# Optimization experiments

Hardware: AMD Instinct MI355X
Metric: run time of the kernel (lower is better)

The kernel has to match this reference:

```python
import jax, jax.numpy as jnp
import numpy as np

D = 64; H = 6; DH = 32; CB = 16; SB = 8; NSEL = 2; WIN = 7; OUT = 7; HID = 32
SCALE = DH ** -0.5
NEG = -3.4e38  # max_neg_value for fp32 masking


def _rope(x):
    # interleaved (lucidrains rotary-embedding-torch style), theta=10000
    n, d = x.shape[-2], x.shape[-1]
    inv = 1.0 / (10000.0 ** (jnp.arange(0, d, 2, dtype=jnp.float32) / d))
    fr = jnp.arange(n, dtype=jnp.float32)[:, None] * inv[None, :]  # n, d/2
    fr = jnp.repeat(fr, 2, axis=-1)                                # n, d
    c, s = jnp.cos(fr), jnp.sin(fr)
    xr = jnp.stack((-x[..., 1::2], x[..., 0::2]), axis=-1).reshape(x.shape)
    return x * c + xr * s


def reference(x, We, be, gamma, Wq, Wk, Wv, k_pos, v_pos, mem_k, mem_v,
              Wkc1, bkc1, Wkc2, bkc2, Wvc1, bvc1, Wvc2, bvc2,
              Wg, bg, Wo, Wh1, bh1, Wh2, bh2):
    B, N = x.shape
    nC = N // CB  # compressed blocks
    nF = N // SB  # fine/selection blocks

    # per-feature scalar embedding: Linear(1, 64)
    h = x[..., None] * We[0] + be  # B,N,D

    # RMSNorm (F.normalize * sqrt(D) * (gamma + 1))
    nrm = jnp.sqrt(jnp.sum(h * h, axis=-1, keepdims=True))
    hn = h / jnp.maximum(nrm, 1e-12) * jnp.sqrt(float(D)) * (gamma + 1.0)

    def proj(W):
        return jnp.einsum('bnd,de->bne', hn, W).reshape(B, N, H, DH).transpose(0, 2, 1, 3)
    q, k, v = proj(Wq), proj(Wk), proj(Wv)  # B,H,N,DH

    # ---- compressed branch (un-rotated q,k; intra-block pos emb + MLP compressor) ----
    kp = jnp.tile(k_pos, (1, nC, 1))  # H,N,DH
    vp = jnp.tile(v_pos, (1, nC, 1))
    CD = CB * DH
    kc_in = (k + kp).reshape(B, H, nC, CD)
    vc_in = (v + vp).reshape(B, H, nC, CD)
    ck = jax.nn.relu(kc_in @ Wkc1 + bkc1) @ Wkc2 + bkc2  # B,H,nC,DH
    cv = jax.nn.relu(vc_in @ Wvc1 + bvc1) @ Wvc2 + bvc2
    ck = jnp.concatenate([jnp.broadcast_to(mem_k, (B, H, 1, DH)), ck], axis=2)
    cv = jnp.concatenate([jnp.broadcast_to(mem_v, (B, H, 1, DH)), cv], axis=2)
    csim = jnp.einsum('bhid,bhjd->bhij', q, ck) * SCALE  # B,H,N,1+nC
    ck_last = jnp.concatenate([jnp.array([-1]), (jnp.arange(nC) + 1) * CB - 1])
    cmask = ck_last[None, :] < jnp.arange(N)[:, None]    # causal: block fully in past (mem kv always visible)
    csim = jnp.where(cmask, csim, NEG)
    c_out = jnp.einsum('bhij,bhjd->bhid', jax.nn.softmax(csim, axis=-1), cv)

    # ---- importance scores -> top-k selection blocks ----
    # compress_block_size != selection_block_size: repeat compressed scores, block-causal mask,
    # mean-pool to selection granularity (uniform within block -> direct mapping), pad+softmax
    rep = CB // SB
    imp = csim[..., 1:][..., jnp.arange(nF) // rep]  # B,H,N,nF
    qb = jnp.arange(N) // SB
    imp = jnp.where(qb[:, None] > jnp.arange(nF)[None, :], imp, NEG)  # strictly-past blocks only
    imp = jnp.concatenate([jnp.full(imp.shape[:-1] + (1,), -1e3, imp.dtype), imp], axis=-1)
    p = jax.nn.softmax(imp, axis=-1)[..., 1:]
    vals, idx = jax.lax.top_k(p, NSEL)  # B,H,N,NSEL

    # rotary only for fine + sliding branches
    qr, kr = _rope(q), _rope(k)

    # ---- fine (selected-block) branch ----
    sel = jnp.concatenate([idx, jnp.broadcast_to(qb[None, None, :, None], (B, H, N, 1))], axis=-1)  # own block appended
    kb = kr.reshape(B, H, nF, SB, DH)
    vb = v.reshape(B, H, nF, SB, DH)
    bi = jnp.arange(B)[:, None, None, None]
    hi = jnp.arange(H)[None, :, None, None]
    fk = kb[bi, hi, sel].reshape(B, H, N, (NSEL + 1) * SB, DH)
    fv = vb[bi, hi, sel].reshape(B, H, N, (NSEL + 1) * SB, DH)
    fmask_sel = jnp.repeat(vals > 1e-10, SB, axis=-1)                     # B,H,N,NSEL*SB
    own = jnp.arange(SB)[None, :] <= (jnp.arange(N) % SB)[:, None]        # causal within own block
    fmask = jnp.concatenate([fmask_sel, jnp.broadcast_to(own, (B, H, N, SB))], axis=-1)
    fsim = jnp.einsum('bhid,bhijd->bhij', qr, fk) * SCALE
    fsim = jnp.where(fmask, fsim, NEG)
    f_out = jnp.einsum('bhij,bhijd->bhid', jax.nn.softmax(fsim, axis=-1), fv)

    off = jnp.arange(WIN + 1)
    kidx = jnp.arange(N)[:, None] - off[None, :]
    valid = kidx >= 0
    kidx = jnp.maximum(kidx, 0)
    sk = kr[:, :, kidx]
    sv = v[:, :, kidx]
    ssim = jnp.einsum('bhid,bhiwd->bhiw', qr, sk) * SCALE
    ssim = jnp.where(valid, ssim, NEG)
    s_out = jnp.einsum('bhiw,bhiwd->bhid', jax.nn.softmax(ssim, axis=-1), sv)

    # ---- sigmoid-gated strategy combine (order: compressed, fine, sliding) ----
    g = jax.nn.sigmoid(jnp.einsum('bnd,de->bne', hn, Wg) + bg).reshape(B, N, H, 3).transpose(0, 2, 1, 3)
    out = g[..., 0:1] * c_out + g[..., 1:2] * f_out + g[..., 2:3] * s_out  # B,H,N,DH
    out = out.transpose(0, 2, 1, 3).reshape(B, N, H * DH) @ Wo             # B,N,D

    # model head: mean-pool over features, MLP
    pooled = out.mean(axis=1)
    hh = jax.nn.gelu(pooled @ Wh1 + bh1, approximate=False)
    return hh @ Wh2 + bh2


def setup_inputs() -> dict:
    key = jax.random.key(0)
    ks = jax.random.split(key, 20)
    B, N = 32, 512
    CD = CB * DH
    f32 = jnp.float32

    def rn(k, shape, fan_in):
        return jax.random.normal(k, shape, f32) / np.sqrt(fan_in)

    return {
        'x': jax.random.normal(ks[0], (B, N), f32),
        'We': rn(ks[1], (1, D), 1),
        'be': jnp.zeros((D,), f32),
        'gamma': 0.1 * jax.random.normal(ks[2], (D,), f32),
        'Wq': rn(ks[3], (D, H * DH), D),
        'Wk': rn(ks[4], (D, H * DH), D),
        'Wv': rn(ks[5], (D, H * DH), D),
        'k_pos': 0.02 * jax.random.normal(ks[6], (H, CB, DH), f32),
        'v_pos': 0.02 * jax.random.normal(ks[7], (H, CB, DH), f32),
        'mem_k': 0.02 * jax.random.normal(ks[8], (H, 1, DH), f32),
        'mem_v': 0.02 * jax.random.normal(ks[9], (H, 1, DH), f32),
        'Wkc1': rn(ks[10], (CD, CD), CD), 'bkc1': jnp.zeros((CD,), f32),
        'Wkc2': rn(ks[11], (CD, DH), CD), 'bkc2': jnp.zeros((DH,), f32),
        'Wvc1': rn(ks[12], (CD, CD), CD), 'bvc1': jnp.zeros((CD,), f32),
        'Wvc2': rn(ks[13], (CD, DH), CD), 'bvc2': jnp.zeros((DH,), f32),
        'Wg': rn(ks[14], (D, 3 * H), D),
        'bg': jnp.tile(jnp.array([-2.0, -2.0, 2.0], f32), H),
        'Wo': rn(ks[15], (H * DH, D), H * DH),
        'Wh1': rn(ks[16], (D, HID), D), 'bh1': jnp.zeros((HID,), f32),
        'Wh2': rn(ks[17], (HID, OUT), HID), 'bh2': jnp.zeros((OUT,), f32),
    }
```

## Files before the change

### kernel.cpp

```cpp
#include <hip/hip_runtime.h>

typedef unsigned short ushort_t;
typedef __attribute__((ext_vector_type(8))) short bf16x8;
typedef __attribute__((ext_vector_type(4))) float f32x4;

constexpr int N_   = 512;
constexpr int D_   = 64;
constexpr int H_   = 6;
constexpr int DH_  = 32;
constexpr int CB_  = 16;
constexpr int SB_  = 8;
constexpr int HD_  = H_ * DH_;
constexpr int CD_  = CB_ * DH_;
constexpr int nC_  = N_ / CB_;
constexpr int nF_  = N_ / SB_;
constexpr float SCALE_ = 0.17677669529663687f;
constexpr float NEG_ = -3.4e38f;

__device__ __forceinline__ ushort_t f2bf(float x) {
    unsigned u = __float_as_uint(x);
    unsigned r = u + 0x7FFFu + ((u >> 16) & 1u);
    return (ushort_t)(r >> 16);
}

__device__ __forceinline__ size_t frag_addr(int row, int k) {
    return (size_t)(row >> 4) * 8192 + (size_t)(k >> 5) * 512
         + (size_t)((k >> 3) & 3) * 128 + (size_t)(row & 15) * 8 + (k & 7);
}

__global__ __launch_bounds__(256) void k_cvtW(
    const float* __restrict__ Wk1, const float* __restrict__ Wv1,
    ushort_t* __restrict__ wtk_hi, ushort_t* __restrict__ wtk_lo,
    ushort_t* __restrict__ wtv_hi, ushort_t* __restrict__ wtv_lo)
{
    const float* W = blockIdx.z ? Wv1 : Wk1;
    ushort_t* ohi = blockIdx.z ? wtv_hi : wtk_hi;
    ushort_t* olo = blockIdx.z ? wtv_lo : wtk_lo;
    const int k0 = blockIdx.x * 64, j0 = blockIdx.y * 64;
    const int t = threadIdx.x;
    __shared__ float tile[64][65];
    #pragma unroll 4
    for (int i = 0; i < 16; ++i) {
        const int lin = t + i * 256;
        const int kk = lin >> 6, jj = lin & 63;
        tile[kk][jj] = W[(size_t)(k0 + kk) * 512 + j0 + jj];
    }
    __syncthreads();
    #pragma unroll 4
    for (int i = 0; i < 16; ++i) {
        const int lin = t + i * 256;
        const int jj = lin >> 6, kk = lin & 63;
        const float x = tile[kk][jj];
        const ushort_t h = f2bf(x);
        const float hf = __uint_as_float((unsigned)h << 16);
        const size_t fo = frag_addr(j0 + jj, k0 + kk);
        ohi[fo] = h;
        olo[fo] = f2bf(x - hf);
    }
}

__global__ __launch_bounds__(192) void k_embed(
    const float* __restrict__ x, const float* __restrict__ We, const float* __restrict__ be,
    const float* __restrict__ gamma,
    const float* __restrict__ Wq, const float* __restrict__ Wk, const float* __restrict__ Wv,
    const float* __restrict__ kpos, const float* __restrict__ vpos,
    const float* __restrict__ Wg, const float* __restrict__ bg,
    float* __restrict__ q, float* __restrict__ qr, float* __restrict__ kr,
    float* __restrict__ v,
    ushort_t* __restrict__ kin_hi, ushort_t* __restrict__ kin_lo,
    ushort_t* __restrict__ vin_hi, ushort_t* __restrict__ vin_lo,
    float* __restrict__ g)
{
    const int t  = threadIdx.x;
    const int wv = t >> 6;
    const int ln = t & 63;
    const int n00 = blockIdx.x * 16;
    const int b = n00 / N_;
    const int nbase = n00 % N_;

    __shared__ float hn[16][64];

    for (int r = wv; r < 16; r += 3) {
        const int n = nbase + r;
        float xv = x[b * N_ + n];
        float h = fmaf(xv, We[ln], be[ln]);
        float ss = h * h;
        #pragma unroll
        for (int off = 32; off; off >>= 1) ss += __shfl_down(ss, off);
        ss = __shfl(ss, 0);
        float sc = 8.0f / fmaxf(sqrtf(ss), 1e-12f);
        hn[r][ln] = h * sc * (gamma[ln] + 1.0f);
    }
    __syncthreads();

    const int e  = ln + (wv << 6);
    const int hh = e >> 5;
    const int dh = e & 31;
    float aq[16], ak[16], av[16];
    #pragma unroll
    for (int r = 0; r < 16; ++r) { aq[r] = 0.f; ak[r] = 0.f; av[r] = 0.f; }
    for (int dd = 0; dd < 64; ++dd) {
        const float wq_ = Wq[dd * HD_ + e];
        const float wk_ = Wk[dd * HD_ + e];
        const float wv_ = Wv[dd * HD_ + e];
        #pragma unroll
        for (int r = 0; r < 16; ++r) {
            const float hv = hn[r][dd];
            aq[r] = fmaf(hv, wq_, aq[r]);
            ak[r] = fmaf(hv, wk_, ak[r]);
            av[r] = fmaf(hv, wv_, av[r]);
        }
    }
    const float invf = exp2f((float)(dh & ~1) * -0.41524101186092029f);
    #pragma unroll
    for (int r = 0; r < 16; ++r) {
        const int n = nbase + r;
        const size_t o = ((size_t)(b * H_ + hh) * N_ + n) * DH_ + dh;
        q[o] = aq[r];
        v[o] = av[r];
        const int pix = (hh * CB_ + (n & (CB_ - 1))) * DH_ + dh;
        const float kinv = ak[r] + kpos[pix];
        const float vinv = av[r] + vpos[pix];
        {
            const int row = (b * H_ + hh) * nC_ + (n >> 4);
            const int k   = (n & 15) * 32 + dh;
            const size_t fo = frag_addr(row, k);
            const ushort_t kh = f2bf(kinv);
            kin_hi[fo] = kh;
            kin_lo[fo] = f2bf(kinv - __uint_as_float((unsigned)kh << 16));
            const ushort_t vh = f2bf(vinv);
            vin_hi[fo] = vh;
            vin_lo[fo] = f2bf(vinv - __uint_as_float((unsigned)vh << 16));
        }
        const float aqp = __shfl_xor(aq[r], 1);
        const float akp = __shfl_xor(ak[r], 1);
        float sA, cA;
        __sincosf((float)n * invf, &sA, &cA);
        float rq, rk;
        if (dh & 1) { rq = fmaf(aqp, sA, aq[r] * cA); rk = fmaf(akp, sA, ak[r] * cA); }
        else        { rq = fmaf(-aqp, sA, aq[r] * cA); rk = fmaf(-akp, sA, ak[r] * cA); }
        qr[o] = rq; kr[o] = rk;
    }

    if (ln < 18) {
        for (int r = wv; r < 16; r += 3) {
            const int n = nbase + r;
            float a = bg[ln];
            for (int dd = 0; dd < 64; ++dd) a = fmaf(hn[r][dd], Wg[dd * 18 + ln], a);
            const float gv = 1.0f / (1.0f + __expf(-a));
            g[((size_t)(b * H_ + ln / 3) * N_ + n) * 3 + (ln % 3)] = gv;
        }
    }
}

__global__ void k_memtok(const float* __restrict__ mk, const float* __restrict__ mv,
                         float* __restrict__ ck, float* __restrict__ cv)
{
    const int bh = blockIdx.x;
    const int h = bh % H_;
    const int t = threadIdx.x;
    ck[(size_t)bh * 33 * DH_ + t] = mk[h * DH_ + t];
    cv[(size_t)bh * 33 * DH_ + t] = mv[h * DH_ + t];
}

__global__ __launch_bounds__(256) void k_compress(
    const ushort_t* __restrict__ kin_hi, const ushort_t* __restrict__ kin_lo,
    const ushort_t* __restrict__ vin_hi, const ushort_t* __restrict__ vin_lo,
    const ushort_t* __restrict__ wtk_hi, const ushort_t* __restrict__ wtk_lo,
    const ushort_t* __restrict__ wtv_hi, const ushort_t* __restrict__ wtv_lo,
    const float* __restrict__ bk1, const float* __restrict__ Wk2, const float* __restrict__ bk2,
    const float* __restrict__ bv1, const float* __restrict__ Wv2, const float* __restrict__ bv2,
    float* __restrict__ ck, float* __restrict__ cv)
{
    const bool isv = blockIdx.y != 0;
    const ushort_t* xhi = isv ? vin_hi : kin_hi;
    const ushort_t* xlo = isv ? vin_lo : kin_lo;
    const ushort_t* whi = isv ? wtv_hi : wtk_hi;
    const ushort_t* wlo = isv ? wtv_lo : wtk_lo;
    const float* b1 = isv ? bv1 : bk1;
    const float* W2 = isv ? Wv2 : Wk2;
    const float* b2 = isv ? bv2 : bk2;
    float* outp = isv ? cv : ck;

    const int row0 = blockIdx.x * 32;
    const int t = threadIdx.x;
    const int w = t >> 6, l = t & 63;
    const int lrow = l & 15, kg = l >> 4;
    const int n0w = w * 128;

    __shared__ float hid[32 * 512];
    __shared__ float wred[4 * 16 * 32];

    f32x4 acc[2][8];
    #pragma unroll
    for (int nt = 0; nt < 8; ++nt) {
        const float bv_ = b1[n0w + nt * 16 + lrow];
        #pragma unroll
        for (int mt = 0; mt < 2; ++mt) {
            acc[mt][nt][0] = bv_; acc[mt][nt][1] = bv_;
            acc[mt][nt][2] = bv_; acc[mt][nt][3] = bv_;
        }
    }
    const ushort_t* Ah = xhi + (size_t)(row0 >> 4) * 8192;
    const ushort_t* Al = xlo + (size_t)(row0 >> 4) * 8192;
    const ushort_t* Bh = whi + (size_t)(n0w >> 4) * 8192;
    const ushort_t* Bl = wlo + (size_t)(n0w >> 4) * 8192;
    const int lofs = l * 8;

    for (int ks = 0; ks < 16; ++ks) {
        const int kb = ks * 512 + lofs;
        const bf16x8 ah0 = *(const bf16x8*)(Ah + kb);
        const bf16x8 ah1 = *(const bf16x8*)(Ah + 8192 + kb);
        const bf16x8 al0 = *(const bf16x8*)(Al + kb);
        const bf16x8 al1 = *(const bf16x8*)(Al + 8192 + kb);
        #pragma unroll
        for (int nt = 0; nt < 8; ++nt) {
            const bf16x8 bh = *(const bf16x8*)(Bh + nt * 8192 + kb);
            const bf16x8 bl = *(const bf16x8*)(Bl + nt * 8192 + kb);
            acc[0][nt] = __builtin_amdgcn_mfma_f32_16x16x32_bf16(ah0, bh, acc[0][nt], 0, 0, 0);
            acc[0][nt] = __builtin_amdgcn_mfma_f32_16x16x32_bf16(ah0, bl, acc[0][nt], 0, 0, 0);
            acc[0][nt] = __builtin_amdgcn_mfma_f32_16x16x32_bf16(al0, bh, acc[0][nt], 0, 0, 0);
            acc[1][nt] = __builtin_amdgcn_mfma_f32_16x16x32_bf16(ah1, bh, acc[1][nt], 0, 0, 0);
            acc[1][nt] = __builtin_amdgcn_mfma_f32_16x16x32_bf16(ah1, bl, acc[1][nt], 0, 0, 0);
            acc[1][nt] = __builtin_amdgcn_mfma_f32_16x16x32_bf16(al1, bh, acc[1][nt], 0, 0, 0);
        }
    }
    #pragma unroll
    for (int mt = 0; mt < 2; ++mt) {
        #pragma unroll
        for (int nt = 0; nt < 8; ++nt) {
            const int col = n0w + nt * 16 + lrow;
            #pragma unroll
            for (int r = 0; r < 4; ++r) {
                const int row = mt * 16 + kg * 4 + r;
                hid[row * 512 + col] = fmaxf(acc[mt][nt][r], 0.0f);
            }
        }
    }
    __syncthreads();

    const int o = t & 31, seg = t >> 5;
    for (int half = 0; half < 2; ++half) {
        const int r0 = half * 16;
        float s[16];
        #pragma unroll
        for (int r = 0; r < 16; ++r) s[r] = 0.f;
        for (int di = 0; di < 64; ++di) {
            const int dd = seg * 64 + di;
            const float w2 = W2[(size_t)dd * 32 + o];
            #pragma unroll
            for (int r = 0; r < 16; ++r) s[r] = fmaf(hid[(r0 + r) * 512 + dd], w2, s[r]);
        }
        #pragma unroll
        for (int r = 0; r < 16; ++r) s[r] += __shfl_xor(s[r], 32);
        if (l < 32) {
            #pragma unroll
            for (int r = 0; r < 16; ++r) wred[(w * 16 + r) * 32 + o] = s[r];
        }
        __syncthreads();
        {
            const int rr = t >> 5;
            #pragma unroll
            for (int u = 0; u < 2; ++u) {
                const int r = rr + u * 8;
                const float val = wred[r * 32 + o] + wred[(16 + r) * 32 + o]
                                + wred[(32 + r) * 32 + o] + wred[(48 + r) * 32 + o] + b2[o];
                const int grow = row0 + r0 + r;
                outp[((size_t)(grow >> 5) * 33 + 1 + (grow & 31)) * DH_ + o] = val;
            }
        }
        __syncthreads();
    }
}

__global__ __launch_bounds__(256) void k_attn(
    const float* __restrict__ q, const float* __restrict__ qr,
    const float* __restrict__ kr, const float* __restrict__ v,
    const float* __restrict__ ck, const float* __restrict__ cv,
    const float* __restrict__ g, float* __restrict__ outb)
{
    const int t = threadIdx.x;
    const int sub = t & 3;
    const int gid = blockIdx.x * 64 + (t >> 2);
    const int n = gid & (N_ - 1);
    const int bh = gid >> 9;
    const int b = bh / H_, h = bh % H_;
    const int qb = n >> 3;

    float qv[8];
    {
        const float4* p = (const float4*)(q + ((size_t)bh * N_ + n) * DH_ + sub * 8);
        const float4 f0 = p[0], f1 = p[1];
        qv[0]=f0.x; qv[1]=f0.y; qv[2]=f0.z; qv[3]=f0.w;
        qv[4]=f1.x; qv[5]=f1.y; qv[6]=f1.z; qv[7]=f1.w;
    }
    const float* ckb = ck + (size_t)bh * 33 * DH_;
    const float* cvb = cv + (size_t)bh * 33 * DH_;

    float mx = -INFINITY, den = 0.f;
    float cres[8];
    #pragma unroll
    for (int d = 0; d < 8; ++d) cres[d] = 0.f;
    float m2 = -1000.0f, sum2 = 1.0f;
    float v1 = -INFINITY, v2 = -INFINITY;
    int i1 = 0, i2 = 0;

    const int jend = 1 + max(n >> 4, (qb + 1) >> 1);
    for (int j = 0; j < jend; ++j) {
        float a = 0.f;
        {
            const float4* kp = (const float4*)(ckb + j * DH_ + sub * 8);
            const float4 f0 = kp[0], f1 = kp[1];
            a = fmaf(qv[0], f0.x, a); a = fmaf(qv[1], f0.y, a);
            a = fmaf(qv[2], f0.z, a); a = fmaf(qv[3], f0.w, a);
            a = fmaf(qv[4], f1.x, a); a = fmaf(qv[5], f1.y, a);
            a = fmaf(qv[6], f1.z, a); a = fmaf(qv[7], f1.w, a);
        }
        a += __shfl_xor(a, 1);
        a += __shfl_xor(a, 2);
        const bool ok = (j == 0) || (j * CB_ - 1 < n);
        a = ok ? a * SCALE_ : NEG_;

        float p;
        if (a > mx) {
            const float sc_ = __expf(mx - a);
            den *= sc_;
            #pragma unroll
            for (int d = 0; d < 8; ++d) cres[d] *= sc_;
            mx = a; p = 1.0f;
        } else {
            p = __expf(a - mx);
        }
        den += p;
        {
            const float4* vp = (const float4*)(cvb + j * DH_ + sub * 8);
            const float4 f0 = vp[0], f1 = vp[1];
            cres[0] = fmaf(p, f0.x, cres[0]); cres[1] = fmaf(p, f0.y, cres[1]);
            cres[2] = fmaf(p, f0.z, cres[2]); cres[3] = fmaf(p, f0.w, cres[3]);
            cres[4] = fmaf(p, f1.x, cres[4]); cres[5] = fmaf(p, f1.y, cres[5]);
            cres[6] = fmaf(p, f1.z, cres[6]); cres[7] = fmaf(p, f1.w, cres[7]);
        }

        if (j >= 1) {
            const int f0i = 2 * (j - 1);
            const int cnt = (qb > f0i) + (qb > f0i + 1);
            if (cnt) {
                if (a > m2) {
                    sum2 = fmaf(sum2, __expf(m2 - a), (float)cnt);
                    m2 = a;
                } else {
                    sum2 = fmaf((float)cnt, __expf(a - m2), sum2);
                }
                if (a > v1) {
                    if (cnt == 2) { v2 = a; i2 = f0i + 1; }
                    else          { v2 = v1; i2 = i1; }
                    v1 = a; i1 = f0i;
                } else if (a > v2) {
                    v2 = a; i2 = f0i;
                }
            }
        }
    }
    {
        const float invd = 1.0f / den;
        #pragma unroll
        for (int d = 0; d < 8; ++d) cres[d] *= invd;
    }
    const float isum = 1.0f / sum2;
    const bool bm0 = __expf(v1 - m2) * isum > 1e-10f;
    const bool bm1 = __expf(v2 - m2) * isum > 1e-10f;

    float qrv[8];
    {
        const float4* p = (const float4*)(qr + ((size_t)bh * N_ + n) * DH_ + sub * 8);
        const float4 f0 = p[0], f1 = p[1];
        qrv[0]=f0.x; qrv[1]=f0.y; qrv[2]=f0.z; qrv[3]=f0.w;
        qrv[4]=f1.x; qrv[5]=f1.y; qrv[6]=f1.z; qrv[7]=f1.w;
    }
    const float* krb = kr + (size_t)bh * N_ * DH_;
    const float* vb  = v  + (size_t)bh * N_ * DH_;

    int blocks[3]; bool bmask[3];
    blocks[0] = i1; blocks[1] = i2; blocks[2] = qb;
    bmask[0] = bm0; bmask[1] = bm1; bmask[2] = true;

    float fmx = -INFINITY, fden = 0.f;
    float fo[8];
    #pragma unroll
    for (int d = 0; d < 8; ++d) fo[d] = 0.f;
    #pragma unroll
    for (int s = 0; s < 3; ++s) {
        const int base = blocks[s] * SB_;
        #pragma unroll
        for (int j = 0; j < 8; ++j) {
            const int row = base + j;
            float a = 0.f;
            {
                const float4* kp = (const float4*)(krb + (size_t)row * DH_ + sub * 8);
                const float4 f0 = kp[0], f1 = kp[1];
                a = fmaf(qrv[0], f0.x, a); a = fmaf(qrv[1], f0.y, a);
                a = fmaf(qrv[2], f0.z, a); a = fmaf(qrv[3], f0.w, a);
                a = fmaf(qrv[4], f1.x, a); a = fmaf(qrv[5], f1.y, a);
                a = fmaf(qrv[6], f1.z, a); a = fmaf(qrv[7], f1.w, a);
            }
            a += __shfl_xor(a, 1);
            a += __shfl_xor(a, 2);
            const bool ok = (s < 2) ? bmask[s] : (j <= (n & 7));
            a = ok ? a * SCALE_ : NEG_;

            float p;
            if (a > fmx) {
                const float sc_ = __expf(fmx - a);
                fden *= sc_;
                #pragma unroll
                for (int d = 0; d < 8; ++d) fo[d] *= sc_;
                fmx = a; p = 1.0f;
            } else {
                p = __expf(a - fmx);
            }
            fden += p;
            const float4* vp = (const float4*)(vb + (size_t)row * DH_ + sub * 8);
            const float4 f0 = vp[0], f1 = vp[1];
            fo[0] = fmaf(p, f0.x, fo[0]); fo[1] = fmaf(p, f0.y, fo[1]);
            fo[2] = fmaf(p, f0.z, fo[2]); fo[3] = fmaf(p, f0.w, fo[3]);
            fo[4] = fmaf(p, f1.x, fo[4]); fo[5] = fmaf(p, f1.y, fo[5]);
            fo[6] = fmaf(p, f1.z, fo[6]); fo[7] = fmaf(p, f1.w, fo[7]);
        }
    }
    const float finv = 1.0f / fden;

    float wmx = -INFINITY, wden = 0.f;
    float so[8];
    #pragma unroll
    for (int d = 0; d < 8; ++d) so[d] = 0.f;
    #pragma unroll
    for (int w = 0; w < 8; ++w) {
        const int row = (n - w) >= 0 ? (n - w) : 0;
        float a;
        if (w <= n) {
            a = 0.f;
            const float4* kp = (const float4*)(krb + (size_t)row * DH_ + sub * 8);
            const float4 f0 = kp[0], f1 = kp[1];
            a = fmaf(qrv[0], f0.x, a); a = fmaf(qrv[1], f0.y, a);
            a = fmaf(qrv[2], f0.z, a); a = fmaf(qrv[3], f0.w, a);
            a = fmaf(qrv[4], f1.x, a); a = fmaf(qrv[5], f1.y, a);
            a = fmaf(qrv[6], f1.z, a); a = fmaf(qrv[7], f1.w, a);
            a += __shfl_xor(a, 1);
            a += __shfl_xor(a, 2);
            a *= SCALE_;
        } else a = NEG_;

        float p;
        if (a > wmx) {
            const float sc_ = __expf(wmx - a);
            wden *= sc_;
            #pragma unroll
            for (int d = 0; d < 8; ++d) so[d] *= sc_;
            wmx = a; p = 1.0f;
        } else {
            p = __expf(a - wmx);
        }
        wden += p;
        const float4* vp = (const float4*)(vb + (size_t)row * DH_ + sub * 8);
        const float4 f0 = vp[0], f1 = vp[1];
        so[0] = fmaf(p, f0.x, so[0]); so[1] = fmaf(p, f0.y, so[1]);
        so[2] = fmaf(p, f0.z, so[2]); so[3] = fmaf(p, f0.w, so[3]);
        so[4] = fmaf(p, f1.x, so[4]); so[5] = fmaf(p, f1.y, so[5]);
        so[6] = fmaf(p, f1.z, so[6]); so[7] = fmaf(p, f1.w, so[7]);
    }
    const float winv = 1.0f / wden;

    const float g0 = g[((size_t)bh * N_ + n) * 3];
    const float g1 = g[((size_t)bh * N_ + n) * 3 + 1];
    const float g2 = g[((size_t)bh * N_ + n) * 3 + 2];
    float4 o0, o1;
    o0.x = g0 * cres[0] + g1 * (fo[0] * finv) + g2 * (so[0] * winv);
    o0.y = g0 * cres[1] + g1 * (fo[1] * finv) + g2 * (so[1] * winv);
    o0.z = g0 * cres[2] + g1 * (fo[2] * finv) + g2 * (so[2] * winv);
    o0.w = g0 * cres[3] + g1 * (fo[3] * finv) + g2 * (so[3] * winv);
    o1.x = g0 * cres[4] + g1 * (fo[4] * finv) + g2 * (so[4] * winv);
    o1.y = g0 * cres[5] + g1 * (fo[5] * finv) + g2 * (so[5] * winv);
    o1.z = g0 * cres[6] + g1 * (fo[6] * finv) + g2 * (so[6] * winv);
    o1.w = g0 * cres[7] + g1 * (fo[7] * finv) + g2 * (so[7] * winv);
    float4* op = (float4*)(outb + ((size_t)(b * N_ + n) * HD_ + h * DH_ + sub * 8));
    op[0] = o0; op[1] = o1;
}

__global__ __launch_bounds__(192) void k_colsum(const float* __restrict__ outb,
                                                float* __restrict__ partial)
{
    const int b = blockIdx.x >> 3, sgm = blockIdx.x & 7;
    const int e = threadIdx.x;
    const int nbase = sgm * 64;
    float s = 0.f;
    for (int nn = 0; nn < 64; ++nn)
        s += outb[((size_t)b * N_ + nbase + nn) * HD_ + e];
    partial[((size_t)b * 8 + sgm) * HD_ + e] = s;
}

__global__ void k_head(const float* __restrict__ partial, const float* __restrict__ Wo,
                       const float* __restrict__ Wh1, const float* __restrict__ bh1,
                       const float* __restrict__ Wh2, const float* __restrict__ bh2,
                       float* __restrict__ out)
{
    const int b = blockIdx.x;
    const int t = threadIdx.x;
    __shared__ float cs[192];
    __shared__ float pooled[64];
    __shared__ float hid[32];
    for (int i = t; i < 192; i += 64) {
        float s = 0.f;
        #pragma unroll
        for (int sg = 0; sg < 8; ++sg) s += partial[((size_t)b * 8 + sg) * HD_ + i];
        cs[i] = s;
    }
    __syncthreads();
    float a = 0.f;
    for (int e = 0; e < 192; ++e) a = fmaf(cs[e], Wo[e * 64 + t], a);
    pooled[t] = a * (1.0f / (float)N_);
    __syncthreads();
    if (t < 32) {
        float s = bh1[t];
        for (int d = 0; d < 64; ++d) s = fmaf(pooled[d], Wh1[d * 32 + t], s);
        hid[t] = 0.5f * s * (1.0f + erff(s * 0.7071067811865476f));
    }
    __syncthreads();
    if (t < 7) {
        float s = bh2[t];
        for (int j = 0; j < 32; ++j) s = fmaf(hid[j], Wh2[j * 7 + t], s);
        out[b * 7 + t] = s;
    }
}

extern "C" void kernel_launch(void* const* d_in, const int* in_sizes, int n_in,
                              void* d_out, int out_size, void* d_ws, size_t ws_size,
                              hipStream_t stream)
{
    const float* x     = (const float*)d_in[0];
    const float* We    = (const float*)d_in[1];
    const float* be    = (const float*)d_in[2];
    const float* gamma = (const float*)d_in[3];
    const float* Wq    = (const float*)d_in[4];
    const float* Wk    = (const float*)d_in[5];
    const float* Wv    = (const float*)d_in[6];
    const float* kpos  = (const float*)d_in[7];
    const float* vpos  = (const float*)d_in[8];
    const float* mk    = (const float*)d_in[9];
    const float* mv    = (const float*)d_in[10];
    const float* Wkc1  = (const float*)d_in[11];
    const float* bkc1  = (const float*)d_in[12];
    const float* Wkc2  = (const float*)d_in[13];
    const float* bkc2  = (const float*)d_in[14];
    const float* Wvc1  = (const float*)d_in[15];
    const float* bvc1  = (const float*)d_in[16];
    const float* Wvc2  = (const float*)d_in[17];
    const float* bvc2  = (const float*)d_in[18];
    const float* Wg    = (const float*)d_in[19];
    const float* bg    = (const float*)d_in[20];
    const float* Wo    = (const float*)d_in[21];
    const float* Wh1   = (const float*)d_in[22];
    const float* bh1   = (const float*)d_in[23];
    const float* Wh2   = (const float*)d_in[24];
    const float* bh2   = (const float*)d_in[25];
    float* out = (float*)d_out;

    const int B = in_sizes[0] / N_;
    const int BH = B * H_;
    const int BHN = BH * N_;
    const size_t SZ = (size_t)BHN * DH_;

    float* ws   = (float*)d_ws;
    float* q_   = ws;
    float* qr_  = ws + SZ;
    float* kr_  = ws + 2 * SZ;
    float* v_   = ws + 3 * SZ;
    ushort_t* kin_hi = (ushort_t*)(ws + 4 * SZ);
    ushort_t* kin_lo = kin_hi + SZ;
    ushort_t* vin_hi = kin_hi + 2 * SZ;
    ushort_t* vin_lo = kin_hi + 3 * SZ;
    float* outb_ = ws + 4 * SZ;
    float* ck_  = ws + 6 * SZ;
    float* cv_  = ck_ + (size_t)BH * 33 * DH_;
    float* g_   = cv_ + (size_t)BH * 33 * DH_;
    float* partial_ = g_ + (size_t)BHN * 3;
    ushort_t* wtk_hi = (ushort_t*)(partial_ + (size_t)B * 8 * HD_);
    ushort_t* wtk_lo = wtk_hi + 512 * 512;
    ushort_t* wtv_hi = wtk_hi + 2 * 512 * 512;
    ushort_t* wtv_lo = wtk_hi + 3 * 512 * 512;

    k_cvtW<<<dim3(8, 8, 2), dim3(256), 0, stream>>>(
        Wkc1, Wvc1, wtk_hi, wtk_lo, wtv_hi, wtv_lo);
    k_embed<<<dim3(B * N_ / 16), dim3(192), 0, stream>>>(
        x, We, be, gamma, Wq, Wk, Wv, kpos, vpos, Wg, bg,
        q_, qr_, kr_, v_, kin_hi, kin_lo, vin_hi, vin_lo, g_);
    k_memtok<<<dim3(BH), dim3(32), 0, stream>>>(mk, mv, ck_, cv_);
    k_compress<<<dim3(BH * nC_ / 32, 2), dim3(256), 0, stream>>>(
        kin_hi, kin_lo, vin_hi, vin_lo, wtk_hi, wtk_lo, wtv_hi, wtv_lo,
        bkc1, Wkc2, bkc2, bvc1, Wvc2, bvc2, ck_, cv_);
    k_attn<<<dim3(BHN / 64), dim3(256), 0, stream>>>(
        q_, qr_, kr_, v_, ck_, cv_, g_, outb_);
    k_colsum<<<dim3(B * 8), dim3(192), 0, stream>>>(outb_, partial_);
    k_head<<<dim3(B), dim3(64), 0, stream>>>(partial_, Wo, Wh1, bh1, Wh2, bh2, out);
}
```

Before: 165.0 us.

## Fuse column-sum into attention and memory-token write into compressor

The attention kernel now reduces its per-query outputs with wave shuffles and shared memory and writes per-(bh,block) partial sums directly. This removes the full outb buffer write and the separate colsum kernel. Query rows are reassigned so each block holds a strided set of positions for one bh, which balances causal work across blocks. Memory-token initialisation moves into k_compress, removing one launch, and the QKV projection loop gets an unroll-4 pragma.

```diff
diff --git a/kernel.cpp b/kernel.cpp
--- a/kernel.cpp
+++ b/kernel.cpp
@@ -99,6 +99,7 @@
     float aq[16], ak[16], av[16];
     #pragma unroll
     for (int r = 0; r < 16; ++r) { aq[r] = 0.f; ak[r] = 0.f; av[r] = 0.f; }
+    #pragma unroll 4
     for (int dd = 0; dd < 64; ++dd) {
         const float wq_ = Wq[dd * HD_ + e];
         const float wk_ = Wk[dd * HD_ + e];
@@ -153,16 +154,6 @@
     }
 }
 
-__global__ void k_memtok(const float* __restrict__ mk, const float* __restrict__ mv,
-                         float* __restrict__ ck, float* __restrict__ cv)
-{
-    const int bh = blockIdx.x;
-    const int h = bh % H_;
-    const int t = threadIdx.x;
-    ck[(size_t)bh * 33 * DH_ + t] = mk[h * DH_ + t];
-    cv[(size_t)bh * 33 * DH_ + t] = mv[h * DH_ + t];
-}
-
 __global__ __launch_bounds__(256) void k_compress(
     const ushort_t* __restrict__ kin_hi, const ushort_t* __restrict__ kin_lo,
     const ushort_t* __restrict__ vin_hi, const ushort_t* __restrict__ vin_lo,
@@ -170,6 +161,7 @@
     const ushort_t* __restrict__ wtv_hi, const ushort_t* __restrict__ wtv_lo,
     const float* __restrict__ bk1, const float* __restrict__ Wk2, const float* __restrict__ bk2,
     const float* __restrict__ bv1, const float* __restrict__ Wv2, const float* __restrict__ bv2,
+    const float* __restrict__ mk, const float* __restrict__ mv,
     float* __restrict__ ck, float* __restrict__ cv)
 {
     const bool isv = blockIdx.y != 0;
@@ -180,6 +172,7 @@
     const float* b1 = isv ? bv1 : bk1;
     const float* W2 = isv ? Wv2 : Wk2;
     const float* b2 = isv ? bv2 : bk2;
+    const float* mtok = isv ? mv : mk;
     float* outp = isv ? cv : ck;
 
     const int row0 = blockIdx.x * 32;
@@ -190,6 +183,10 @@
 
     __shared__ float hid[32 * 512];
     __shared__ float wred[4 * 16 * 32];
+
+    if (t < 32) {
+        outp[(size_t)blockIdx.x * 33 * DH_ + t] = mtok[(blockIdx.x % H_) * DH_ + t];
+    }
 
     f32x4 acc[2][8];
     #pragma unroll
@@ -277,15 +274,17 @@
     const float* __restrict__ q, const float* __restrict__ qr,
     const float* __restrict__ kr, const float* __restrict__ v,
     const float* __restrict__ ck, const float* __restrict__ cv,
-    const float* __restrict__ g, float* __restrict__ outb)
+    const float* __restrict__ g, float* __restrict__ partial)
 {
     const int t = threadIdx.x;
     const int sub = t & 3;
-    const int gid = blockIdx.x * 64 + (t >> 2);
-    const int n = gid & (N_ - 1);
-    const int bh = gid >> 9;
-    const int b = bh / H_, h = bh % H_;
-    const int qb = n >> 3;
+    const int wv = t >> 6;
+    const int l = t & 63;
+    const int bh = blockIdx.x >> 3;
+    const int blk = blockIdx.x & 7;
+    const int qi = ((l >> 2) << 2) + wv;
+    const int n = blk + (qi << 3);
+    const int qb = qi;
 
     float qv[8];
     {
@@ -473,29 +472,28 @@
     const float g0 = g[((size_t)bh * N_ + n) * 3];
     const float g1 = g[((size_t)bh * N_ + n) * 3 + 1];
     const float g2 = g[((size_t)bh * N_ + n) * 3 + 2];
-    float4 o0, o1;
-    o0.x = g0 * cres[0] + g1 * (fo[0] * finv) + g2 * (so[0] * winv);
-    o0.y = g0 * cres[1] + g1 * (fo[1] * finv) + g2 * (so[1] * winv);
-    o0.z = g0 * cres[2] + g1 * (fo[2] * finv) + g2 * (so[2] * winv);
-    o0.w = g0 * cres[3] + g1 * (fo[3] * finv) + g2 * (so[3] * winv);
-    o1.x = g0 * cres[4] + g1 * (fo[4] * finv) + g2 * (so[4] * winv);
-    o1.y = g0 * cres[5] + g1 * (fo[5] * finv) + g2 * (so[5] * winv);
-    o1.z = g0 * cres[6] + g1 * (fo[6] * finv) + g2 * (so[6] * winv);
-    o1.w = g0 * cres[7] + g1 * (fo[7] * finv) + g2 * (so[7] * winv);
-    float4* op = (float4*)(outb + ((size_t)(b * N_ + n) * HD_ + h * DH_ + sub * 8));
-    op[0] = o0; op[1] = o1;
-}
-
-__global__ __launch_bounds__(192) void k_colsum(const float* __restrict__ outb,
-                                                float* __restrict__ partial)
-{
-    const int b = blockIdx.x >> 3, sgm = blockIdx.x & 7;
-    const int e = threadIdx.x;
-    const int nbase = sgm * 64;
-    float s = 0.f;
-    for (int nn = 0; nn < 64; ++nn)
-        s += outb[((size_t)b * N_ + nbase + nn) * HD_ + e];
-    partial[((size_t)b * 8 + sgm) * HD_ + e] = s;
+    float o[8];
+    #pragma unroll
+    for (int d = 0; d < 8; ++d)
+        o[d] = g0 * cres[d] + g1 * (fo[d] * finv) + g2 * (so[d] * winv);
+
+    #pragma unroll
+    for (int d = 0; d < 8; ++d) {
+        o[d] += __shfl_down(o[d], 32);
+        o[d] += __shfl_down(o[d], 16);
+        o[d] += __shfl_down(o[d], 8);
+        o[d] += __shfl_down(o[d], 4);
+    }
+    __shared__ float red[4][32];
+    if (l < 4) {
+        #pragma unroll
+        for (int d = 0; d < 8; ++d) red[wv][l * 8 + d] = o[d];
+    }
+    __syncthreads();
+    if (t < 32) {
+        const float s = red[0][t] + red[1][t] + red[2][t] + red[3][t];
+        partial[((size_t)bh * 8 + blk) * 32 + t] = s;
+    }
 }
 
 __global__ void k_head(const float* __restrict__ partial, const float* __restrict__ Wo,
@@ -509,9 +507,11 @@
     __shared__ float pooled[64];
     __shared__ float hid[32];
     for (int i = t; i < 192; i += 64) {
+        const int h = i >> 5, dh = i & 31;
         float s = 0.f;
         #pragma unroll
-        for (int sg = 0; sg < 8; ++sg) s += partial[((size_t)b * 8 + sg) * HD_ + i];
+        for (int sg = 0; sg < 8; ++sg)
+            s += partial[(((size_t)(b * H_ + h)) * 8 + sg) * 32 + dh];
         cs[i] = s;
     }
     __syncthreads();
@@ -578,12 +578,11 @@
     ushort_t* kin_lo = kin_hi + SZ;
     ushort_t* vin_hi = kin_hi + 2 * SZ;
     ushort_t* vin_lo = kin_hi + 3 * SZ;
-    float* outb_ = ws + 4 * SZ;
     float* ck_  = ws + 6 * SZ;
     float* cv_  = ck_ + (size_t)BH * 33 * DH_;
     float* g_   = cv_ + (size_t)BH * 33 * DH_;
     float* partial_ = g_ + (size_t)BHN * 3;
-    ushort_t* wtk_hi = (ushort_t*)(partial_ + (size_t)B * 8 * HD_);
+    ushort_t* wtk_hi = (ushort_t*)(partial_ + (size_t)BH * 8 * 32);
     ushort_t* wtk_lo = wtk_hi + 512 * 512;
     ushort_t* wtv_hi = wtk_hi + 2 * 512 * 512;
     ushort_t* wtv_lo = wtk_hi + 3 * 512 * 512;
@@ -593,12 +592,10 @@
     k_embed<<<dim3(B * N_ / 16), dim3(192), 0, stream>>>(
         x, We, be, gamma, Wq, Wk, Wv, kpos, vpos, Wg, bg,
         q_, qr_, kr_, v_, kin_hi, kin_lo, vin_hi, vin_lo, g_);
-    k_memtok<<<dim3(BH), dim3(32), 0, stream>>>(mk, mv, ck_, cv_);
-    k_compress<<<dim3(BH * nC_ / 32, 2), dim3(256), 0, stream>>>(
+    k_compress<<<dim3(BH, 2), dim3(256), 0, stream>>>(
         kin_hi, kin_lo, vin_hi, vin_lo, wtk_hi, wtk_lo, wtv_hi, wtv_lo,
-        bkc1, Wkc2, bkc2, bvc1, Wvc2, bvc2, ck_, cv_);
+        bkc1, Wkc2, bkc2, bvc1, Wvc2, bvc2, mk, mv, ck_, cv_);
     k_attn<<<dim3(BHN / 64), dim3(256), 0, stream>>>(
-        q_, qr_, kr_, v_, ck_, cv_, g_, outb_);
-    k_colsum<<<dim3(B * 8), dim3(192), 0, stream>>>(outb_, partial_);
+        q_, qr_, kr_, v_, ck_, cv_, g_, partial_);
     k_head<<<dim3(B), dim3(64), 0, stream>>>(partial_, Wo, Wh1, bh1, Wh2, bh2, out);
 }
```

New measurement: 215.7 us. +30.7%, slower.
